# Performance work log

Hardware: AMD Instinct MI355X
Metric: run time of the kernel (lower is better)

## Reference

```python
import jax, jax.numpy as jnp
import numpy as np

N = 65536
INPUT_DIM = 768
OUTPUT_DIM = 256
NUM_LEVELS = 4
CODEBOOK_SIZE = 1024
BETA = 0.25
LN_EPS = 1e-5


def setup_inputs() -> dict:
    key = jax.random.key(0)
    ks = jax.random.split(key, 12)
    s_in = 1.0 / np.sqrt(INPUT_DIM)
    s_out = 1.0 / np.sqrt(OUTPUT_DIM)
    return {
        "x": jax.random.normal(ks[0], (N, INPUT_DIM), dtype=jnp.float32),
        "ln_g": jnp.ones((INPUT_DIM,), dtype=jnp.float32),
        "ln_b": jnp.zeros((INPUT_DIM,), dtype=jnp.float32),
        # weights stored [in, out] (torch Linear is [out, in]); math identical
        "W1": jax.random.uniform(ks[1], (INPUT_DIM, OUTPUT_DIM), jnp.float32, -s_in, s_in),
        "b1": jax.random.uniform(ks[2], (OUTPUT_DIM,), jnp.float32, -s_in, s_in),
        "W2": jax.random.uniform(ks[3], (OUTPUT_DIM, OUTPUT_DIM), jnp.float32, -s_out, s_out),
        "b2": jax.random.uniform(ks[4], (OUTPUT_DIM,), jnp.float32, -s_out, s_out),
        "Wd1": jax.random.uniform(ks[5], (OUTPUT_DIM, INPUT_DIM), jnp.float32, -s_out, s_out),
        "bd1": jax.random.uniform(ks[6], (INPUT_DIM,), jnp.float32, -s_out, s_out),
        "Wd2": jax.random.uniform(ks[7], (INPUT_DIM, INPUT_DIM), jnp.float32, -s_in, s_in),
        "bd2": jax.random.uniform(ks[8], (INPUT_DIM,), jnp.float32, -s_in, s_in),
        "codebooks": jax.random.normal(ks[9], (NUM_LEVELS, CODEBOOK_SIZE, OUTPUT_DIM), dtype=jnp.float32),
    }


def _quantize_with_loss(enc, codebooks):
    residual = enc
    q_final = jnp.zeros_like(enc)
    commit = jnp.float32(0.0)
    indices = []
    for l in range(NUM_LEVELS):
        cb = codebooks[l]  # [K, D]
        # squared euclidean distance: ||r||^2 - 2 r.c + ||c||^2 -> [N, K]
        d = (jnp.sum(residual ** 2, axis=1, keepdims=True)
             - 2.0 * residual @ cb.T
             + jnp.sum(cb ** 2, axis=1)[None, :])
        idx = jnp.argmin(d, axis=1)  # [N]
        indices.append(idx)
        q = cb[idx]  # [N, D]
        commit = commit + jnp.mean((jax.lax.stop_gradient(residual) - q) ** 2)
        q_final = q_final + q
        q_st = residual + jax.lax.stop_gradient(q - residual)  # straight-through
        residual = residual - q_st
    return q_final, jnp.stack(indices, axis=1), commit


def reference(x, ln_g, ln_b, W1, b1, W2, b2, Wd1, bd1, Wd2, bd2, codebooks):
    # encoder: LayerNorm -> Linear -> ReLU -> Linear
    mu = jnp.mean(x, axis=-1, keepdims=True)
    var = jnp.mean((x - mu) ** 2, axis=-1, keepdims=True)
    xn = (x - mu) * jax.lax.rsqrt(var + LN_EPS) * ln_g + ln_b
    enc = jax.nn.relu(xn @ W1 + b1) @ W2 + b2  # [N, D]

    q, indices, commit = _quantize_with_loss(enc, codebooks)

    # decoder: Linear -> ReLU -> Linear
    recon = jax.nn.relu(q @ Wd1 + bd1) @ Wd2 + bd2  # [N, input_dim]

    rec_loss = jnp.mean((recon - x) ** 2)
    loss = rec_loss + BETA * commit
    return loss, recon, indices
```

## Files before the change

kernel.cpp:

```cpp
#include <hip/hip_runtime.h>
#include <hip/hip_bf16.h>
#include <stdint.h>

#define NROWS 65536
#define INDIM 768
#define ODIM  256
#define NLEV  4
#define CBS   1024
#define TAUQ  2e-2f

typedef __attribute__((ext_vector_type(8))) short short8;
typedef __attribute__((ext_vector_type(4))) float f32x4;

__device__ __forceinline__ float bf2f(unsigned short u) {
    union { unsigned int i; float f; } v; v.i = ((unsigned int)u) << 16; return v.f;
}
__device__ __forceinline__ unsigned short f2bf(float f) {
    union { float f; unsigned int i; } v; v.f = f;
    unsigned int r = v.i + 0x7fffu + ((v.i >> 16) & 1u);
    return (unsigned short)(r >> 16);
}
__device__ __forceinline__ f32x4 mfma_bf16(short8 a, short8 b, f32x4 c) {
    return __builtin_amdgcn_mfma_f32_16x16x32_bf16(a, b, c, 0, 0, 0);
}

__global__ void k_init(double* __restrict__ acc) {
    if (threadIdx.x < 2) acc[threadIdx.x] = 0.0;
}

__global__ __launch_bounds__(64) void k_cnorm(const float* __restrict__ cb, float* __restrict__ cn) {
    const int code = blockIdx.x;
    const float* r = cb + (size_t)code * ODIM + threadIdx.x * 4;
    float4 v = *(const float4*)r;
    float s = fmaf(v.x, v.x, fmaf(v.y, v.y, fmaf(v.z, v.z, v.w * v.w)));
    #pragma unroll
    for (int o = 32; o > 0; o >>= 1) s += __shfl_xor(s, o);
    if (threadIdx.x == 0) cn[code] = s;
}

__global__ __launch_bounds__(256) void k_split(const float* __restrict__ cb,
                                               unsigned short* __restrict__ ch,
                                               unsigned short* __restrict__ cl) {
    const size_t i = ((size_t)blockIdx.x * 256 + threadIdx.x) * 4;
    float4 v = *(const float4*)(cb + i);
    float e[4] = {v.x, v.y, v.z, v.w};
    ushort4 h, l;
    unsigned short* hp = &h.x; unsigned short* lp = &l.x;
    #pragma unroll
    for (int j = 0; j < 4; ++j) {
        unsigned short hh = f2bf(e[j]);
        hp[j] = hh;
        lp[j] = f2bf(e[j] - bf2f(hh));
    }
    *(ushort4*)(ch + i) = h;
    *(ushort4*)(cl + i) = l;
}

__global__ __launch_bounds__(256) void k_cbt(const float* __restrict__ cb, float* __restrict__ ct) {
    __shared__ float T[32][33];
    const int l  = blockIdx.z;
    const int c0 = blockIdx.x << 5;
    const int k0 = blockIdx.y << 5;
    const int tx = threadIdx.x & 31, ty = threadIdx.x >> 5;
    const float* src = cb + ((size_t)l * CBS + c0) * ODIM + k0;
    #pragma unroll
    for (int i = 0; i < 4; ++i)
        T[ty + (i << 3)][tx] = src[(size_t)(ty + (i << 3)) * ODIM + tx];
    __syncthreads();
    float* dst = ct + ((size_t)l * ODIM + k0) * CBS + c0;
    #pragma unroll
    for (int i = 0; i < 4; ++i)
        dst[(size_t)(ty + (i << 3)) * CBS + tx] = T[tx][ty + (i << 3)];
}

__global__ __launch_bounds__(256) void k_wt(const float* __restrict__ W,
                                            unsigned short* __restrict__ Th,
                                            unsigned short* __restrict__ Tl,
                                            const int K, const int N, const int split) {
    const int n = blockIdx.x;
    for (int k = threadIdx.x; k < K; k += 256) {
        float v = W[(size_t)k * N + n];
        unsigned short h = f2bf(v);
        Th[(size_t)n * K + k] = h;
        if (split) Tl[(size_t)n * K + k] = f2bf(v - bf2f(h));
    }
}

__global__ __launch_bounds__(256) void k_ln(const float* __restrict__ x,
                                            float* __restrict__ mu, float* __restrict__ rsig) {
    const int row = blockIdx.x;
    const int t = threadIdx.x;
    const float* xr = x + (size_t)row * INDIM;
    float a = xr[t], b = xr[t + 256], c = xr[t + 512];
    float s1 = a + b + c;
    float s2 = fmaf(a, a, fmaf(b, b, c * c));
    #pragma unroll
    for (int o = 32; o > 0; o >>= 1) { s1 += __shfl_xor(s1, o); s2 += __shfl_xor(s2, o); }
    __shared__ float r1[4], r2[4];
    if ((t & 63) == 0) { r1[t >> 6] = s1; r2[t >> 6] = s2; }
    __syncthreads();
    if (t == 0) {
        float S1 = (r1[0] + r1[1]) + (r1[2] + r1[3]);
        float S2 = (r2[0] + r2[1]) + (r2[2] + r2[3]);
        float m = S1 * (1.0f / INDIM);
        float var = S2 * (1.0f / INDIM) - m * m;
        mu[row] = m;
        rsig[row] = rsqrtf(var + 1e-5f);
    }
}

template <int AMODE, int SPLIT, int EPI>
__global__ __attribute__((amdgpu_flat_work_group_size(256, 256), amdgpu_waves_per_eu(2, 2)))
void k_gemm_mfma(
    const void* __restrict__ Ap, const unsigned short* __restrict__ Bh,
    const unsigned short* __restrict__ Bl,
    const float* __restrict__ bias, void* __restrict__ Cp,
    const int K, const int Nc,
    const float* __restrict__ mu, const float* __restrict__ rsig,
    const float* __restrict__ lng, const float* __restrict__ lnb,
    const float* __restrict__ xref, double* __restrict__ acc_rec)
{
    __shared__ __align__(16) unsigned short BhS[256][40];
    __shared__ __align__(16) unsigned short BlS[SPLIT ? 256 : 8][SPLIT ? 40 : 8];
    __shared__ float credsh[4];

    const int t = threadIdx.x;
    const int wave = t >> 6, lane = t & 63;
    const int lg = lane >> 4, lm = lane & 15;
    const int wm = wave >> 1, wn = wave & 1;
    const size_t rowb = (size_t)blockIdx.y * 128 + wm * 64;
    const int nb = blockIdx.x << 8;

    f32x4 acc[4][8];
    #pragma unroll
    for (int mt = 0; mt < 4; ++mt)
        #pragma unroll
        for (int nt = 0; nt < 8; ++nt) acc[mt][nt] = (f32x4){0.f, 0.f, 0.f, 0.f};

    float lnm[4], lnr[4];
    if (AMODE == 1) {
        #pragma unroll
        for (int mt = 0; mt < 4; ++mt) {
            lnm[mt] = mu[rowb + (mt << 4) + lm];
            lnr[mt] = rsig[rowb + (mt << 4) + lm];
        }
    }

    for (int kk = 0; kk < K; kk += 32) {
        short8 Ah[4], Al[4];
        if (AMODE == 2) {
            #pragma unroll
            for (int mt = 0; mt < 4; ++mt)
                Ah[mt] = *(const short8*)((const unsigned short*)Ap +
                          (rowb + (mt << 4) + lm) * (size_t)K + kk + (lg << 3));
        } else {
            float g[8], bb[8];
            if (AMODE == 1) {
                float4 g0 = *(const float4*)(lng + kk + (lg << 3));
                float4 g1 = *(const float4*)(lng + kk + (lg << 3) + 4);
                float4 b0 = *(const float4*)(lnb + kk + (lg << 3));
                float4 b1 = *(const float4*)(lnb + kk + (lg << 3) + 4);
                g[0]=g0.x; g[1]=g0.y; g[2]=g0.z; g[3]=g0.w; g[4]=g1.x; g[5]=g1.y; g[6]=g1.z; g[7]=g1.w;
                bb[0]=b0.x; bb[1]=b0.y; bb[2]=b0.z; bb[3]=b0.w; bb[4]=b1.x; bb[5]=b1.y; bb[6]=b1.z; bb[7]=b1.w;
            }
            #pragma unroll
            for (int mt = 0; mt < 4; ++mt) {
                const float* ar = (const float*)Ap + (rowb + (mt << 4) + lm) * (size_t)K + kk + (lg << 3);
                float4 a0 = *(const float4*)ar;
                float4 a1 = *(const float4*)(ar + 4);
                float e[8] = {a0.x, a0.y, a0.z, a0.w, a1.x, a1.y, a1.z, a1.w};
                #pragma unroll
                for (int j = 0; j < 8; ++j) {
                    float v = e[j];
                    if (AMODE == 1) v = fmaf((v - lnm[mt]) * lnr[mt], g[j], bb[j]);
                    unsigned short h = f2bf(v);
                    Ah[mt][j] = (short)h;
                    Al[mt][j] = (short)f2bf(v - bf2f(h));
                }
            }
        }
        __syncthreads();
        {
            const unsigned short* gh = Bh + (size_t)nb * K + kk;
            #pragma unroll
            for (int it = 0; it < 4; ++it) {
                const int idx = (it << 8) + t;
                const int n = idx >> 2, sl = idx & 3;
                *(uint4*)&BhS[n][sl << 3] = *(const uint4*)(gh + (size_t)n * K + (sl << 3));
            }
            if (SPLIT) {
                const unsigned short* gl = Bl + (size_t)nb * K + kk;
                #pragma unroll
                for (int it = 0; it < 4; ++it) {
                    const int idx = (it << 8) + t;
                    const int n = idx >> 2, sl = idx & 3;
                    *(uint4*)&BlS[n][sl << 3] = *(const uint4*)(gl + (size_t)n * K + (sl << 3));
                }
            }
        }
        __syncthreads();
        #pragma unroll
        for (int nt = 0; nt < 8; ++nt) {
            const int nl = (wn << 7) + (nt << 4) + lm;
            short8 bh = *(const short8*)&BhS[nl][lg << 3];
            if (!SPLIT) {
                #pragma unroll
                for (int mt = 0; mt < 4; ++mt)
                    acc[mt][nt] = mfma_bf16(Ah[mt], bh, acc[mt][nt]);
            } else {
                short8 bl = *(const short8*)&BlS[nl][lg << 3];
                #pragma unroll
                for (int mt = 0; mt < 4; ++mt) {
                    acc[mt][nt] = mfma_bf16(Ah[mt], bh, acc[mt][nt]);
                    acc[mt][nt] = mfma_bf16(Al[mt], bh, acc[mt][nt]);
                    acc[mt][nt] = mfma_bf16(Ah[mt], bl, acc[mt][nt]);
                }
            }
        }
    }

    float lsum = 0.0f;
    #pragma unroll
    for (int nt = 0; nt < 8; ++nt) {
        const int col = nb + (wn << 7) + (nt << 4) + lm;
        const float bs = bias[col];
        #pragma unroll
        for (int mt = 0; mt < 4; ++mt) {
            #pragma unroll
            for (int r = 0; r < 4; ++r) {
                float v = acc[mt][nt][r] + bs;
                if (EPI == 0 || EPI == 2) v = fmaxf(v, 0.0f);
                const size_t row = rowb + (mt << 4) + (lg << 2) + r;
                if (EPI == 2) {
                    ((unsigned short*)Cp)[row * Nc + col] = f2bf(v);
                } else {
                    ((float*)Cp)[row * Nc + col] = v;
                }
                if (EPI == 3) {
                    const float d = v - xref[row * Nc + col];
                    lsum = fmaf(d, d, lsum);
                }
            }
        }
    }
    if (EPI == 3) {
        #pragma unroll
        for (int o = 32; o > 0; o >>= 1) lsum += __shfl_xor(lsum, o);
        if (lane == 0) credsh[wave] = lsum;
        __syncthreads();
        if (t == 0) atomicAdd(acc_rec, (double)((credsh[0] + credsh[1]) + (credsh[2] + credsh[3])));
    }
}

__global__ __attribute__((amdgpu_flat_work_group_size(256, 256), amdgpu_waves_per_eu(2, 2)))
void k_quant_mfma(
    const float* __restrict__ enc, const float* __restrict__ cb,
    const unsigned short* __restrict__ cbh, const unsigned short* __restrict__ cbl,
    const float* __restrict__ cnorm, unsigned short* __restrict__ qf, float* __restrict__ oidx,
    int* __restrict__ flag, double* __restrict__ acc_commit)
{
    __shared__ __align__(16) unsigned short Bh[32][264];
    __shared__ __align__(16) unsigned short Bl[32][264];
    __shared__ __align__(16) int rowidxsh[128];
    __shared__ float credsh[4];

    const int t = threadIdx.x;
    const int wave = t >> 6, lane = t & 63;
    const int lg = lane >> 4, lm = lane & 15;
    const size_t rowbase = (size_t)blockIdx.x * 128 + wave * 32;

    short8 Ah[2][8], Al[2][8];
    #pragma unroll
    for (int mt = 0; mt < 2; ++mt)
        #pragma unroll
        for (int s = 0; s < 8; ++s) {
            const float* er = enc + (rowbase + mt * 16 + lm) * ODIM + s * 32 + lg * 8;
            float4 e0 = *(const float4*)er;
            float4 e1 = *(const float4*)(er + 4);
            float e[8] = {e0.x, e0.y, e0.z, e0.w, e1.x, e1.y, e1.z, e1.w};
            #pragma unroll
            for (int j = 0; j < 8; ++j) {
                unsigned short h = f2bf(e[j]);
                Ah[mt][s][j] = (short)h;
                Al[mt][s][j] = (short)f2bf(e[j] - bf2f(h));
            }
        }

    float commit_local = 0.0f;
    int flg[2][4] = {{0, 0, 0, 0}, {0, 0, 0, 0}};

    for (int l = 0; l < NLEV; ++l) {
        const size_t lbase = (size_t)l * CBS * ODIM;
        float bestv[2][4], b2v[2][4];
        int besti[2][4];
        #pragma unroll
        for (int mt = 0; mt < 2; ++mt)
            #pragma unroll
            for (int r = 0; r < 4; ++r) { bestv[mt][r] = 3.4e38f; b2v[mt][r] = 3.4e38f; besti[mt][r] = 0; }

        for (int ch = 0; ch < 32; ++ch) {
            const int cbase = ch << 5;
            __syncthreads();
            {
                const unsigned short* gh = cbh + lbase + (size_t)cbase * ODIM;
                const unsigned short* gl = cbl + lbase + (size_t)cbase * ODIM;
                #pragma unroll
                for (int r = 0; r < 4; ++r) {
                    const int i = (r << 8) + t;
                    const int code = i >> 5, sl = i & 31;
                    *(uint4*)&Bh[code][sl << 3] = *(const uint4*)(gh + ((size_t)i << 3));
                    *(uint4*)&Bl[code][sl << 3] = *(const uint4*)(gl + ((size_t)i << 3));
                }
            }
            __syncthreads();
            #pragma unroll
            for (int nt = 0; nt < 2; ++nt) {
                f32x4 p0[2], p1[2];
                #pragma unroll
                for (int mt = 0; mt < 2; ++mt) {
                    p0[mt] = (f32x4){0.f, 0.f, 0.f, 0.f};
                    p1[mt] = (f32x4){0.f, 0.f, 0.f, 0.f};
                }
                #pragma unroll
                for (int s = 0; s < 8; ++s) {
                    short8 bh = *(const short8*)&Bh[(nt << 4) + lm][(s << 5) + (lg << 3)];
                    short8 bl = *(const short8*)&Bl[(nt << 4) + lm][(s << 5) + (lg << 3)];
                    p0[0] = mfma_bf16(Ah[0][s], bh, p0[0]);
                    p0[1] = mfma_bf16(Ah[1][s], bh, p0[1]);
                    p1[0] = mfma_bf16(Al[0][s], bh, p1[0]);
                    p1[1] = mfma_bf16(Al[1][s], bh, p1[1]);
                    p1[0] = mfma_bf16(Ah[0][s], bl, p1[0]);
                    p1[1] = mfma_bf16(Ah[1][s], bl, p1[1]);
                }
                const int code = cbase + (nt << 4) + lm;
                const float cn = cnorm[(l << 10) + code];
                #pragma unroll
                for (int mt = 0; mt < 2; ++mt)
                    #pragma unroll
                    for (int r = 0; r < 4; ++r) {
                        const float d = fmaf(-2.0f, p0[mt][r] + p1[mt][r], cn);
                        if (d < bestv[mt][r]) {
                            b2v[mt][r] = bestv[mt][r]; bestv[mt][r] = d; besti[mt][r] = code;
                        } else {
                            b2v[mt][r] = fminf(b2v[mt][r], d);
                        }
                    }
            }
        }

        #pragma unroll
        for (int mt = 0; mt < 2; ++mt) {
            int iv[4];
            #pragma unroll
            for (int r = 0; r < 4; ++r) {
                float bv = bestv[mt][r], b2 = b2v[mt][r];
                int bi = besti[mt][r];
                #pragma unroll
                for (int off = 1; off < 16; off <<= 1) {
                    float ov = __shfl_xor(bv, off);
                    float o2 = __shfl_xor(b2, off);
                    int   oi = __shfl_xor(bi, off);
                    if (ov < bv)      { b2 = fminf(bv, o2); bv = ov; bi = oi; }
                    else if (ov > bv) { b2 = fminf(b2, ov); }
                    else              { b2 = bv; bi = (oi < bi) ? oi : bi; }
                }
                flg[mt][r] |= (b2 - bv < TAUQ) ? 1 : 0;
                iv[r] = bi;
                if (lm == 0)
                    oidx[(rowbase + (mt << 4) + (lg << 2) + r) * NLEV + l] = (float)bi;
            }
            if (lm == 0)
                *(int4*)&rowidxsh[(wave << 5) + (mt << 4) + (lg << 2)] = make_int4(iv[0], iv[1], iv[2], iv[3]);
        }
        __syncthreads();

        #pragma unroll
        for (int mt = 0; mt < 2; ++mt) {
            const int ci = rowidxsh[(wave << 5) + (mt << 4) + lm];
            const float* cr = cb + lbase + (size_t)ci * ODIM + lg * 8;
            #pragma unroll
            for (int s = 0; s < 8; ++s) {
                float4 c0 = *(const float4*)(cr + (s << 5));
                float4 c1 = *(const float4*)(cr + (s << 5) + 4);
                float c[8] = {c0.x, c0.y, c0.z, c0.w, c1.x, c1.y, c1.z, c1.w};
                #pragma unroll
                for (int j = 0; j < 8; ++j) {
                    float rr = bf2f((unsigned short)Ah[mt][s][j]) + bf2f((unsigned short)Al[mt][s][j]) - c[j];
                    commit_local = fmaf(rr, rr, commit_local);
                    unsigned short h = f2bf(rr);
                    Ah[mt][s][j] = (short)h;
                    Al[mt][s][j] = (short)f2bf(rr - bf2f(h));
                }
            }
        }
    }

    #pragma unroll
    for (int mt = 0; mt < 2; ++mt)
        #pragma unroll
        for (int s = 0; s < 8; ++s) {
            const size_t ro = (rowbase + mt * 16 + lm) * ODIM + s * 32 + lg * 8;
            float4 e0 = *(const float4*)(enc + ro);
            float4 e1 = *(const float4*)(enc + ro + 4);
            float e[8] = {e0.x, e0.y, e0.z, e0.w, e1.x, e1.y, e1.z, e1.w};
            unsigned short q[8];
            #pragma unroll
            for (int j = 0; j < 8; ++j)
                q[j] = f2bf(e[j] - (bf2f((unsigned short)Ah[mt][s][j]) + bf2f((unsigned short)Al[mt][s][j])));
            *(ushort4*)(qf + ro)     = make_ushort4(q[0], q[1], q[2], q[3]);
            *(ushort4*)(qf + ro + 4) = make_ushort4(q[4], q[5], q[6], q[7]);
        }

    if (lm == 0) {
        #pragma unroll
        for (int mt = 0; mt < 2; ++mt)
            #pragma unroll
            for (int r = 0; r < 4; ++r)
                flag[rowbase + (mt << 4) + (lg << 2) + r] = flg[mt][r];
    }

    #pragma unroll
    for (int o = 32; o > 0; o >>= 1) commit_local += __shfl_xor(commit_local, o);
    if (lane == 0) credsh[wave] = commit_local;
    __syncthreads();
    if (t == 0) atomicAdd(acc_commit, (double)((credsh[0] + credsh[1]) + (credsh[2] + credsh[3])));
}

__global__ __launch_bounds__(256) void k_fix(
    const int* __restrict__ flag, const float* __restrict__ x,
    const float* __restrict__ lng, const float* __restrict__ lnb,
    const float* __restrict__ W1, const float* __restrict__ b1,
    const float* __restrict__ W2, const float* __restrict__ b2,
    const float* __restrict__ cb, const float* __restrict__ ct,
    float* __restrict__ oidx)
{
    const int row = blockIdx.x;
    if (!flag[row]) return;
    const int t = threadIdx.x;
    __shared__ double xn[INDIM];
    __shared__ double hs[ODIM];
    __shared__ double r[ODIM];
    __shared__ double rv_[4];
    __shared__ int ri_[4];
    __shared__ int selidx;

    const float* xr = x + (size_t)row * INDIM;
    double xa = (double)xr[t], xb = (double)xr[t + 256], xc = (double)xr[t + 512];
    double s1 = xa + xb + xc;
    double s2 = xa * xa + xb * xb + xc * xc;
    #pragma unroll
    for (int o = 32; o > 0; o >>= 1) { s1 += __shfl_xor(s1, o); s2 += __shfl_xor(s2, o); }
    __shared__ double w1r[4], w2r[4];
    if ((t & 63) == 0) { w1r[t >> 6] = s1; w2r[t >> 6] = s2; }
    __syncthreads();
    double S1 = (w1r[0] + w1r[1]) + (w1r[2] + w1r[3]);
    double S2 = (w2r[0] + w2r[1]) + (w2r[2] + w2r[3]);
    double mu = S1 / (double)INDIM;
    double var = S2 / (double)INDIM - mu * mu;
    double rs = 1.0 / sqrt(var + 1e-5);
    xn[t]       = (xa - mu) * rs * (double)lng[t]       + (double)lnb[t];
    xn[t + 256] = (xb - mu) * rs * (double)lng[t + 256] + (double)lnb[t + 256];
    xn[t + 512] = (xc - mu) * rs * (double)lng[t + 512] + (double)lnb[t + 512];
    __syncthreads();
    {
        double a0 = 0.0, a1 = 0.0, a2 = 0.0, a3 = 0.0;
        for (int k = 0; k < INDIM; k += 4) {
            a0 = fma(xn[k + 0], (double)W1[(size_t)(k + 0) * ODIM + t], a0);
            a1 = fma(xn[k + 1], (double)W1[(size_t)(k + 1) * ODIM + t], a1);
            a2 = fma(xn[k + 2], (double)W1[(size_t)(k + 2) * ODIM + t], a2);
            a3 = fma(xn[k + 3], (double)W1[(size_t)(k + 3) * ODIM + t], a3);
        }
        hs[t] = fmax(((a0 + a1) + (a2 + a3)) + (double)b1[t], 0.0);
    }
    __syncthreads();
    {
        double a0 = 0.0, a1 = 0.0, a2 = 0.0, a3 = 0.0;
        for (int k = 0; k < ODIM; k += 4) {
            a0 = fma(hs[k + 0], (double)W2[(size_t)(k + 0) * ODIM + t], a0);
            a1 = fma(hs[k + 1], (double)W2[(size_t)(k + 1) * ODIM + t], a1);
            a2 = fma(hs[k + 2], (double)W2[(size_t)(k + 2) * ODIM + t], a2);
            a3 = fma(hs[k + 3], (double)W2[(size_t)(k + 3) * ODIM + t], a3);
        }
        r[t] = ((a0 + a1) + (a2 + a3)) + (double)b2[t];
    }
    __syncthreads();

    for (int l = 0; l < NLEV; ++l) {
        const float* ctl = ct + (size_t)l * CBS * ODIM;
        double d0 = 0.0, d1 = 0.0, d2 = 0.0, d3 = 0.0;
        #pragma unroll 4
        for (int k = 0; k < ODIM; ++k) {
            const double rk = r[k];
            const float4 c4 = *(const float4*)(ctl + ((size_t)k << 10) + (t << 2));
            const double f0 = rk - (double)c4.x;
            const double f1 = rk - (double)c4.y;
            const double f2 = rk - (double)c4.z;
            const double f3 = rk - (double)c4.w;
            d0 = fma(f0, f0, d0); d1 = fma(f1, f1, d1);
            d2 = fma(f2, f2, d2); d3 = fma(f3, f3, d3);
        }
        double bv = d0; int bi = (t << 2);
        if (d1 < bv) { bv = d1; bi = (t << 2) + 1; }
        if (d2 < bv) { bv = d2; bi = (t << 2) + 2; }
        if (d3 < bv) { bv = d3; bi = (t << 2) + 3; }
        #pragma unroll
        for (int o = 32; o > 0; o >>= 1) {
            double ov = __shfl_xor(bv, o);
            int oi = __shfl_xor(bi, o);
            if (ov < bv || (ov == bv && oi < bi)) { bv = ov; bi = oi; }
        }
        if ((t & 63) == 0) { rv_[t >> 6] = bv; ri_[t >> 6] = bi; }
        __syncthreads();
        if (t == 0) {
            double fv = rv_[0]; int fi = ri_[0];
            #pragma unroll
            for (int w = 1; w < 4; ++w)
                if (rv_[w] < fv || (rv_[w] == fv && ri_[w] < fi)) { fv = rv_[w]; fi = ri_[w]; }
            selidx = fi;
            oidx[(size_t)row * NLEV + l] = (float)fi;
        }
        __syncthreads();
        r[t] = r[t] - (double)cb[(size_t)l * CBS * ODIM + (size_t)selidx * ODIM + t];
        __syncthreads();
    }
}

__global__ void k_fin(const double* __restrict__ acc, float* __restrict__ out) {
    if (threadIdx.x == 0)
        out[0] = (float)(acc[1] / ((double)NROWS * (double)INDIM) +
                         0.25 * (acc[0] / ((double)NROWS * (double)ODIM)));
}

extern "C" void kernel_launch(void* const* d_in, const int* in_sizes, int n_in,
                              void* d_out, int out_size, void* d_ws, size_t ws_size,
                              hipStream_t stream)
{
    const float* x   = (const float*)d_in[0];
    const float* lng = (const float*)d_in[1];
    const float* lnb = (const float*)d_in[2];
    const float* W1  = (const float*)d_in[3];
    const float* b1  = (const float*)d_in[4];
    const float* W2  = (const float*)d_in[5];
    const float* b2  = (const float*)d_in[6];
    const float* Wd1 = (const float*)d_in[7];
    const float* bd1 = (const float*)d_in[8];
    const float* Wd2 = (const float*)d_in[9];
    const float* bd2 = (const float*)d_in[10];
    const float* cbs = (const float*)d_in[11];

    char* ws = (char*)d_ws;
    const size_t MB = 1u << 20;
    const size_t O_ACC  = 0;
    const size_t O_CN   = 1024;
    const size_t O_MU   = O_CN + 16384;
    const size_t O_RS   = O_MU + (size_t)NROWS * 4;
    const size_t O_FLAG = O_RS + (size_t)NROWS * 4;
    const size_t O_ENC  = 1 * MB;
    const size_t O_QF   = 65 * MB;
    const size_t O_W1H  = 97 * MB;
    const size_t O_W1L  = O_W1H + (size_t)INDIM * ODIM * 2;
    const size_t O_W2H  = O_W1L + (size_t)INDIM * ODIM * 2;
    const size_t O_W2L  = O_W2H + (size_t)ODIM * ODIM * 2;
    const size_t O_WD1  = O_W2L + (size_t)ODIM * ODIM * 2;
    const size_t O_WD2  = O_WD1 + (size_t)ODIM * INDIM * 2;
    const size_t O_CBH  = 100 * MB;
    const size_t O_CBL  = 102 * MB;
    const size_t O_H1   = 104 * MB;
    const size_t O_CT   = O_H1;

    double* acc   = (double*)(ws + O_ACC);
    float* cnorm  = (float*)(ws + O_CN);
    float* mu     = (float*)(ws + O_MU);
    float* rsig   = (float*)(ws + O_RS);
    int*   flag   = (int*)(ws + O_FLAG);
    float* enc    = (float*)(ws + O_ENC);
    unsigned short* qf  = (unsigned short*)(ws + O_QF);
    unsigned short* w1h = (unsigned short*)(ws + O_W1H);
    unsigned short* w1l = (unsigned short*)(ws + O_W1L);
    unsigned short* w2h = (unsigned short*)(ws + O_W2H);
    unsigned short* w2l = (unsigned short*)(ws + O_W2L);
    unsigned short* wd1h = (unsigned short*)(ws + O_WD1);
    unsigned short* wd2h = (unsigned short*)(ws + O_WD2);
    unsigned short* cbh = (unsigned short*)(ws + O_CBH);
    unsigned short* cbl = (unsigned short*)(ws + O_CBL);
    float* h1     = (float*)(ws + O_H1);
    float* ct     = (float*)(ws + O_CT);
    unsigned short* hd = (unsigned short*)(ws + O_H1);

    float* outF  = (float*)d_out;
    float* recon = outF + 1;
    float* oidx  = outF + 1 + (size_t)NROWS * INDIM;

    k_init<<<1, 64, 0, stream>>>(acc);
    k_cnorm<<<NLEV * CBS, 64, 0, stream>>>(cbs, cnorm);
    k_ln<<<NROWS, 256, 0, stream>>>(x, mu, rsig);
    k_wt<<<ODIM, 256, 0, stream>>>(W1, w1h, w1l, INDIM, ODIM, 1);
    k_wt<<<ODIM, 256, 0, stream>>>(W2, w2h, w2l, ODIM, ODIM, 1);
    k_wt<<<INDIM, 256, 0, stream>>>(Wd1, wd1h, nullptr, ODIM, INDIM, 0);
    k_wt<<<INDIM, 256, 0, stream>>>(Wd2, wd2h, nullptr, INDIM, INDIM, 0);
    k_split<<<(NLEV * CBS * ODIM) / 1024, 256, 0, stream>>>(cbs, cbh, cbl);
    k_gemm_mfma<1, 1, 0><<<dim3(1, NROWS / 128), 256, 0, stream>>>(
        x, w1h, w1l, b1, h1, INDIM, ODIM, mu, rsig, lng, lnb, nullptr, nullptr);
    k_gemm_mfma<0, 1, 1><<<dim3(1, NROWS / 128), 256, 0, stream>>>(
        h1, w2h, w2l, b2, enc, ODIM, ODIM, nullptr, nullptr, nullptr, nullptr, nullptr, nullptr);
    k_cbt<<<dim3(32, 8, 4), 256, 0, stream>>>(cbs, ct);
    k_quant_mfma<<<NROWS / 128, 256, 0, stream>>>(enc, cbs, cbh, cbl, cnorm, qf, oidx, flag, acc);
    k_fix<<<NROWS, 256, 0, stream>>>(flag, x, lng, lnb, W1, b1, W2, b2, cbs, ct, oidx);
    k_gemm_mfma<2, 0, 2><<<dim3(INDIM / 256, NROWS / 128), 256, 0, stream>>>(
        qf, wd1h, nullptr, bd1, hd, ODIM, INDIM, nullptr, nullptr, nullptr, nullptr, nullptr, nullptr);
    k_gemm_mfma<2, 0, 3><<<dim3(INDIM / 256, NROWS / 128), 256, 0, stream>>>(
        hd, wd2h, nullptr, bd2, recon, INDIM, INDIM, nullptr, nullptr, nullptr, nullptr, x, acc + 1);
    k_fin<<<1, 64, 0, stream>>>(acc, outF);
}
```

Baseline: 1.946 ms.

## Load codebook fragments directly from global memory in quantizer, drop LDS staging

```diff
diff --git a/kernel.cpp b/kernel.cpp
--- a/kernel.cpp
+++ b/kernel.cpp
@@ -110,8 +110,7 @@
 }
 
 template <int AMODE, int SPLIT, int EPI>
-__global__ __attribute__((amdgpu_flat_work_group_size(256, 256), amdgpu_waves_per_eu(2, 2)))
-void k_gemm_mfma(
+__global__ __launch_bounds__(256, 2) void k_gemm_mfma(
     const void* __restrict__ Ap, const unsigned short* __restrict__ Bh,
     const unsigned short* __restrict__ Bl,
     const float* __restrict__ bias, void* __restrict__ Cp,
@@ -252,16 +251,12 @@
     }
 }
 
-__global__ __attribute__((amdgpu_flat_work_group_size(256, 256), amdgpu_waves_per_eu(2, 2)))
-void k_quant_mfma(
+__global__ __launch_bounds__(256, 2) void k_quant_mfma(
     const float* __restrict__ enc, const float* __restrict__ cb,
     const unsigned short* __restrict__ cbh, const unsigned short* __restrict__ cbl,
     const float* __restrict__ cnorm, unsigned short* __restrict__ qf, float* __restrict__ oidx,
     int* __restrict__ flag, double* __restrict__ acc_commit)
 {
-    __shared__ __align__(16) unsigned short Bh[32][264];
-    __shared__ __align__(16) unsigned short Bl[32][264];
-    __shared__ __align__(16) int rowidxsh[128];
     __shared__ float credsh[4];
 
     const int t = threadIdx.x;
@@ -300,21 +295,11 @@
 
         for (int ch = 0; ch < 32; ++ch) {
             const int cbase = ch << 5;
-            __syncthreads();
-            {
-                const unsigned short* gh = cbh + lbase + (size_t)cbase * ODIM;
-                const unsigned short* gl = cbl + lbase + (size_t)cbase * ODIM;
-                #pragma unroll
-                for (int r = 0; r < 4; ++r) {
-                    const int i = (r << 8) + t;
-                    const int code = i >> 5, sl = i & 31;
-                    *(uint4*)&Bh[code][sl << 3] = *(const uint4*)(gh + ((size_t)i << 3));
-                    *(uint4*)&Bl[code][sl << 3] = *(const uint4*)(gl + ((size_t)i << 3));
-                }
-            }
-            __syncthreads();
             #pragma unroll
             for (int nt = 0; nt < 2; ++nt) {
+                const int code = cbase + (nt << 4) + lm;
+                const unsigned short* gh = cbh + lbase + (size_t)code * ODIM + (lg << 3);
+                const unsigned short* gl = cbl + lbase + (size_t)code * ODIM + (lg << 3);
                 f32x4 p0[2], p1[2];
                 #pragma unroll
                 for (int mt = 0; mt < 2; ++mt) {
@@ -323,8 +308,8 @@
                 }
                 #pragma unroll
                 for (int s = 0; s < 8; ++s) {
-                    short8 bh = *(const short8*)&Bh[(nt << 4) + lm][(s << 5) + (lg << 3)];
-                    short8 bl = *(const short8*)&Bl[(nt << 4) + lm][(s << 5) + (lg << 3)];
+                    short8 bh = *(const short8*)(gh + (s << 5));
+                    short8 bl = *(const short8*)(gl + (s << 5));
                     p0[0] = mfma_bf16(Ah[0][s], bh, p0[0]);
                     p0[1] = mfma_bf16(Ah[1][s], bh, p0[1]);
                     p1[0] = mfma_bf16(Al[0][s], bh, p1[0]);
@@ -332,7 +317,6 @@
                     p1[0] = mfma_bf16(Ah[0][s], bl, p1[0]);
                     p1[1] = mfma_bf16(Ah[1][s], bl, p1[1]);
                 }
-                const int code = cbase + (nt << 4) + lm;
                 const float cn = cnorm[(l << 10) + code];
                 #pragma unroll
                 for (int mt = 0; mt < 2; ++mt)
@@ -348,6 +332,7 @@
             }
         }
 
+        int ci_sel[2];
         #pragma unroll
         for (int mt = 0; mt < 2; ++mt) {
             int iv[4];
@@ -369,15 +354,18 @@
                 if (lm == 0)
                     oidx[(rowbase + (mt << 4) + (lg << 2) + r) * NLEV + l] = (float)bi;
             }
-            if (lm == 0)
-                *(int4*)&rowidxsh[(wave << 5) + (mt << 4) + (lg << 2)] = make_int4(iv[0], iv[1], iv[2], iv[3]);
-        }
-        __syncthreads();
+            const int srcl = (lm >> 2) << 4;
+            const int t0 = __shfl(iv[0], srcl);
+            const int t1 = __shfl(iv[1], srcl);
+            const int t2 = __shfl(iv[2], srcl);
+            const int t3 = __shfl(iv[3], srcl);
+            const int rr = lm & 3;
+            ci_sel[mt] = (rr == 0) ? t0 : (rr == 1) ? t1 : (rr == 2) ? t2 : t3;
+        }
 
         #pragma unroll
         for (int mt = 0; mt < 2; ++mt) {
-            const int ci = rowidxsh[(wave << 5) + (mt << 4) + lm];
-            const float* cr = cb + lbase + (size_t)ci * ODIM + lg * 8;
+            const float* cr = cb + lbase + (size_t)ci_sel[mt] * ODIM + lg * 8;
             #pragma unroll
             for (int s = 0; s < 8; ++s) {
                 float4 c0 = *(const float4*)(cr + (s << 5));
```

Result: slower. 2.314 ms (+18.9%).
